# Performance work log

Hardware: AMD Instinct MI355X
Metric: run time of the kernel (lower is better)

Reference implementation:

```python
import jax, jax.numpy as jnp
import numpy as np

EMBED = 1024
HEADS = 16
HEAD_DIM = EMBED // HEADS


def setup_inputs() -> dict:
    key = jax.random.key(0)
    ks = jax.random.split(key, 9)
    s = 1.0 / np.sqrt(EMBED)
    inp = {
        "x": jax.random.normal(ks[0], (2, 2048, EMBED), dtype=jnp.float32),
        "wq": jax.random.uniform(ks[1], (EMBED, EMBED), jnp.float32, -s, s),
        "bq": jax.random.uniform(ks[2], (EMBED,), jnp.float32, -s, s),
        "wk": jax.random.uniform(ks[3], (EMBED, EMBED), jnp.float32, -s, s),
        "bk": jax.random.uniform(ks[4], (EMBED,), jnp.float32, -s, s),
        "wv": jax.random.uniform(ks[5], (EMBED, EMBED), jnp.float32, -s, s),
        "bv": jax.random.uniform(ks[6], (EMBED,), jnp.float32, -s, s),
        "wo": jax.random.uniform(ks[7], (EMBED, EMBED), jnp.float32, -s, s),
        "bo": jax.random.uniform(ks[8], (EMBED,), jnp.float32, -s, s),
    }
    return inp


def reference(x, wq, bq, wk, bk, wv, bv, wo, bo):
    B, S, E = x.shape
    H, D = HEADS, HEAD_DIM
    # projections (torch Linear: y = x @ W.T + b; here weights stored as [E, E] applied as x @ W.T)
    q = (x @ wq.T + bq).reshape(B, S, H, D).transpose(0, 2, 1, 3)  # [B,H,S,D]
    k = (x @ wk.T + bk).reshape(B, S, H, D).transpose(0, 2, 1, 3)
    v = (x @ wv.T + bv).reshape(B, S, H, D).transpose(0, 2, 1, 3)
    scores = jnp.einsum("bhqd,bhkd->bhqk", q, k) / jnp.sqrt(jnp.asarray(D, x.dtype))
    attn = jax.nn.softmax(scores, axis=-1)  # dropout is identity in eval / p=0
    ctx = jnp.einsum("bhqk,bhkd->bhqd", attn, v)
    ctx = ctx.transpose(0, 2, 1, 3).reshape(B, S, E)
    return ctx @ wo.T + bo
```

## Files before the change

kernel.cpp:

```cpp
#include <hip/hip_runtime.h>
#include <hip/hip_bf16.h>

#define EMBED 1024
#define HEADS 16
#define HDIM  64
#define BATCH 2
#define SEQ   2048
#define MTOT  (BATCH*SEQ)

typedef __attribute__((ext_vector_type(8))) short bf16x8;
typedef __attribute__((ext_vector_type(4))) short bf16x4;
typedef __attribute__((ext_vector_type(4))) float f32x4;
typedef __attribute__((ext_vector_type(8))) unsigned short u16x8;
typedef __attribute__((ext_vector_type(2))) unsigned u32x2;
typedef __attribute__((ext_vector_type(4))) unsigned u32x4;

__device__ __forceinline__ unsigned pack2(float lo, float hi) {
    __hip_bfloat162 h = __float22bfloat162_rn(make_float2(lo, hi));
    unsigned u;
    __builtin_memcpy(&u, &h, sizeof(u));
    return u;
}
__device__ __forceinline__ unsigned short f2bf(float f) {
    __hip_bfloat16 h = __float2bfloat16(f);
    unsigned short u;
    __builtin_memcpy(&u, &h, sizeof(u));
    return u;
}

__device__ __forceinline__ void glds16(const void* g, void* l) {
    __builtin_amdgcn_global_load_lds(
        (const __attribute__((address_space(1))) void*)g,
        (__attribute__((address_space(3))) void*)l, 16, 0, 0);
}

__global__ __launch_bounds__(256) void preconvert(
    const float* __restrict__ x,
    const float* __restrict__ wq, const float* __restrict__ wk,
    const float* __restrict__ wv, const float* __restrict__ wo,
    unsigned short* __restrict__ xb,
    unsigned short* __restrict__ wqb, unsigned short* __restrict__ wkb,
    unsigned short* __restrict__ wvb, unsigned short* __restrict__ wob)
{
    const int NX = (MTOT * EMBED) / 4;
    const int NW = (EMBED * EMBED) / 4;
    int idx = blockIdx.x * 256 + threadIdx.x;
    const float* src;
    unsigned short* dst;
    int off;
    if (idx < NX) {
        src = x; dst = xb; off = idx;
    } else {
        int r = idx - NX;
        int w = r / NW;
        off = r - w * NW;
        src = (w == 0) ? wq : (w == 1) ? wk : (w == 2) ? wv : wo;
        dst = (w == 0) ? wqb : (w == 1) ? wkb : (w == 2) ? wvb : wob;
    }
    float4 v = ((const float4*)src)[off];
    u32x2 o;
    o[0] = pack2(v.x, v.y);
    o[1] = pack2(v.z, v.w);
    *(u32x2*)(dst + (size_t)off * 4) = o;
}

__global__ __launch_bounds__(256, 2) void qkv_proj(
    const unsigned short* __restrict__ xb,
    const unsigned short* __restrict__ wqb, const float* __restrict__ bq,
    const unsigned short* __restrict__ wkb, const float* __restrict__ bk,
    const unsigned short* __restrict__ wvb, const float* __restrict__ bv,
    unsigned short* __restrict__ qo,
    unsigned short* __restrict__ ko,
    unsigned short* __restrict__ vto)
{
    const int which = blockIdx.z;
    const unsigned short* __restrict__ w =
        (which == 0) ? wqb : (which == 1) ? wkb : wvb;
    const float* __restrict__ bias = (which == 0) ? bq : (which == 1) ? bk : bv;
    const float kscale = (which == 1) ? 0.18033688f : 1.0f;

    const int m0 = blockIdx.x * 128;
    const int n0 = blockIdx.y * 128;

    __shared__ __align__(16) unsigned short a_lds[128 * 32];
    __shared__ __align__(16) unsigned short b_lds[128 * 32];

    const int tid  = threadIdx.x;
    const int lane = tid & 63;
    const int wid  = tid >> 6;
    const int wr   = wid >> 1, wc = wid & 1;
    const int lq   = lane & 15;
    const int lg   = lane >> 4;

    f32x4 acc[4][4] = {};

    const int srow  = wid * 32 + (lane >> 2);
    const int scol8 = (lane & 3) * 8;
    const unsigned short* ap0 = xb + (size_t)(m0 + srow)      * EMBED + scol8;
    const unsigned short* ap1 = xb + (size_t)(m0 + srow + 16) * EMBED + scol8;
    const unsigned short* bp0 = w  + (size_t)(n0 + srow)      * EMBED + scol8;
    const unsigned short* bp1 = w  + (size_t)(n0 + srow + 16) * EMBED + scol8;
    unsigned short* la0 = a_lds + wid * 1024;
    unsigned short* la1 = a_lds + wid * 1024 + 512;
    unsigned short* lb0 = b_lds + wid * 1024;
    unsigned short* lb1 = b_lds + wid * 1024 + 512;

    for (int k0 = 0; k0 < EMBED; k0 += 32) {
        glds16(ap0 + k0, la0);
        glds16(ap1 + k0, la1);
        glds16(bp0 + k0, lb0);
        glds16(bp1 + k0, lb1);
        __syncthreads();
        bf16x8 af[4], bfr[4];
        #pragma unroll
        for (int i = 0; i < 4; ++i)
            af[i] = *(const bf16x8*)&a_lds[(wr*64 + i*16 + lq) * 32 + lg*8];
        #pragma unroll
        for (int j = 0; j < 4; ++j)
            bfr[j] = *(const bf16x8*)&b_lds[(wc*64 + j*16 + lq) * 32 + lg*8];
        #pragma unroll
        for (int i = 0; i < 4; ++i)
            #pragma unroll
            for (int j = 0; j < 4; ++j)
                acc[i][j] = __builtin_amdgcn_mfma_f32_16x16x32_bf16(af[i], bfr[j], acc[i][j], 0, 0, 0);
        __syncthreads();
    }

    #pragma unroll
    for (int j = 0; j < 4; ++j) {
        const int nn = n0 + wc*64 + j*16 + lq;
        const float bsv = bias[nn];
        const int h = nn >> 6, d = nn & (HDIM-1);
        #pragma unroll
        for (int i = 0; i < 4; ++i) {
            const int mmb = m0 + wr*64 + i*16 + lg*4;
            const int b = mmb >> 11;
            const int s = mmb & (SEQ-1);
            const size_t bh = (size_t)(b*HEADS + h);
            if (which == 2) {
                u32x2 ov;
                ov[0] = pack2(acc[i][j][0] + bsv, acc[i][j][1] + bsv);
                ov[1] = pack2(acc[i][j][2] + bsv, acc[i][j][3] + bsv);
                *(u32x2*)&vto[(bh*HDIM + d)*SEQ + s] = ov;
            } else {
                unsigned short* o = (which == 0) ? qo : ko;
                #pragma unroll
                for (int r = 0; r < 4; ++r)
                    o[(bh*SEQ + (s + r))*HDIM + d] = f2bf((acc[i][j][r] + bsv) * kscale);
            }
        }
    }
}

__global__ __launch_bounds__(256, 4) void attn(
    const unsigned short* __restrict__ q,
    const unsigned short* __restrict__ k,
    const unsigned short* __restrict__ vt,
    unsigned short* __restrict__ ctx)
{
    __shared__ __align__(16) unsigned char sm[2 * 16384];

    const int bid   = blockIdx.x;
    const int xcd   = bid & 7;
    const int local = bid >> 3;
    const int bh    = xcd * 4 + (local >> 5);
    const int q0    = (local & 31) * 64;
    const int b     = bh >> 4;
    const int h     = bh & (HEADS - 1);
    const int tid   = threadIdx.x;
    const int wv    = tid >> 6;
    const int lane  = tid & 63;
    const int lq = lane & 15, lg = lane >> 4;

    const unsigned short* qb = q  + (size_t)bh * SEQ * HDIM;
    const unsigned short* kb = k  + (size_t)bh * SEQ * HDIM;
    const unsigned short* vb = vt + (size_t)bh * HDIM * SEQ;

    const int lg16 = lg * 16;
    const int Sp = (((lq & 3) | (((lq >> 2) & 1) << 2)) << 4);
    const int Tp = (((lq & 3) | (((lq >> 3) & 1) << 2)) << 4);
    const int kreadA = (8*(lq >> 2) + (lq & 3)) * 128 + (lg16 ^ Sp);
    const int kreadB = kreadA ^ 64;
    const int vreadA = lq * 128 + (lg16 ^ Tp);
    const int vreadB = vreadA ^ 64;

    const int wrow = tid >> 3;
    const int c8   = tid & 7;
    const int wS   = (((wrow & 3) | (((wrow >> 3) & 1) << 2)) << 4);
    const int woff = wrow * 128 + ((c8 * 16) ^ wS);

    const int scol = c8 * 8;
    const unsigned short* kp = kb + (size_t)wrow * HDIM + scol;
    const unsigned short* vp = vb + (size_t)wrow * SEQ + scol;

    bf16x8 qf[2];
    #pragma unroll
    for (int hh = 0; hh < 2; ++hh)
        qf[hh] = *(const bf16x8*)(qb + (size_t)(q0 + wv*16 + lq) * HDIM + hh*32 + lg*8);

    f32x4 o[4] = {};
    float lr = 0.f;

    u16x8 kr0, kr1, vr0, vr1;

#define LOADT() do {                                                           \
    kr0 = *(const u16x8*)(kp);                                                 \
    kr1 = *(const u16x8*)(kp + 32*HDIM);                                       \
    vr0 = *(const u16x8*)(vp);                                                 \
    vr1 = *(const u16x8*)(vp + 32*SEQ);                                        \
} while (0)

#define WRITET(BF) do {                                                        \
    unsigned char* smb = sm + (BF)*16384;                                      \
    *(u16x8*)(smb +         woff) = kr0;                                       \
    *(u16x8*)(smb +  4096 + woff) = kr1;                                       \
    *(u16x8*)(smb +  8192 + woff) = vr0;                                       \
    *(u16x8*)(smb + 12288 + woff) = vr1;                                       \
} while (0)

#define COMPUTE(BF) do {                                                       \
    const unsigned char* smb = sm + (BF)*16384;                                \
    f32x4 s_[4];                                                               \
    _Pragma("unroll")                                                          \
    for (int sub = 0; sub < 4; ++sub) {                                        \
        const int sadd = (sub & 1) * 512 + (sub >> 1) * 4096;                  \
        bf16x8 k0 = *(const bf16x8*)(smb + sadd + kreadA);                     \
        bf16x8 k1 = *(const bf16x8*)(smb + sadd + kreadB);                     \
        f32x4 z = {};                                                          \
        z = __builtin_amdgcn_mfma_f32_16x16x32_bf16(k0, qf[0], z, 0, 0, 0);    \
        z = __builtin_amdgcn_mfma_f32_16x16x32_bf16(k1, qf[1], z, 0, 0, 0);    \
        s_[sub] = z;                                                           \
    }                                                                          \
    u32x4 pbw0, pbw1;                                                          \
    float psum = 0.f;                                                          \
    _Pragma("unroll")                                                          \
    for (int sub = 0; sub < 4; ++sub) {                                        \
        f32x4 pv;                                                              \
        _Pragma("unroll")                                                      \
        for (int r = 0; r < 4; ++r) pv[r] = exp2f(s_[sub][r]);                 \
        psum += (pv[0] + pv[1]) + (pv[2] + pv[3]);                             \
        unsigned d0 = pack2(pv[0], pv[1]);                                     \
        unsigned d1 = pack2(pv[2], pv[3]);                                     \
        if (sub == 0)      { pbw0[0] = d0; pbw0[1] = d1; }                     \
        else if (sub == 1) { pbw0[2] = d0; pbw0[3] = d1; }                     \
        else if (sub == 2) { pbw1[0] = d0; pbw1[1] = d1; }                     \
        else               { pbw1[2] = d0; pbw1[3] = d1; }                     \
    }                                                                          \
    lr += psum;                                                                \
    bf16x8 pb0 = __builtin_bit_cast(bf16x8, pbw0);                             \
    bf16x8 pb1 = __builtin_bit_cast(bf16x8, pbw1);                             \
    _Pragma("unroll")                                                          \
    for (int i = 0; i < 4; ++i) {                                              \
        bf16x8 va = *(const bf16x8*)(smb + 8192 + i*2048 + vreadA);            \
        bf16x8 vbq = *(const bf16x8*)(smb + 8192 + i*2048 + vreadB);           \
        o[i] = __builtin_amdgcn_mfma_f32_16x16x32_bf16(va,  pb0, o[i], 0, 0, 0); \
        o[i] = __builtin_amdgcn_mfma_f32_16x16x32_bf16(vbq, pb1, o[i], 0, 0, 0); \
    }                                                                          \
} while (0)

    LOADT();
    WRITET(0);
    __syncthreads();
    kp += 64 * HDIM;
    vp += 64;

    for (int t2 = 0; t2 < 16; ++t2) {
        {
            const int t = 2 * t2;
            if (t < 31) LOADT();
            COMPUTE(0);
            if (t < 31) {
                WRITET(1);
                __syncthreads();
                kp += 64 * HDIM;
                vp += 64;
            }
        }
        {
            const int t = 2 * t2 + 1;
            if (t < 31) LOADT();
            COMPUTE(1);
            if (t < 31) {
                WRITET(0);
                __syncthreads();
                kp += 64 * HDIM;
                vp += 64;
            }
        }
    }

#undef LOADT
#undef WRITET
#undef COMPUTE

    float lm = lr + __shfl_xor(lr, 16);
    lm += __shfl_xor(lm, 32);
    const float inv = 1.0f / lm;
    unsigned short* cb = ctx + ((size_t)(b*SEQ + q0 + wv*16 + lq)) * EMBED + h*HDIM;
    #pragma unroll
    for (int i = 0; i < 4; ++i) {
        u32x2 ov;
        ov[0] = pack2(o[i][0] * inv, o[i][1] * inv);
        ov[1] = pack2(o[i][2] * inv, o[i][3] * inv);
        *(u32x2*)(cb + i*16 + lg*4) = ov;
    }
}

__global__ __launch_bounds__(256, 2) void out_proj(
    const unsigned short* __restrict__ ctx,
    const unsigned short* __restrict__ wob, const float* __restrict__ bo,
    float* __restrict__ out)
{
    const int m0 = blockIdx.x * 128;
    const int n0 = blockIdx.y * 128;

    __shared__ __align__(16) unsigned short a_lds[128 * 32];
    __shared__ __align__(16) unsigned short b_lds[128 * 32];

    const int tid  = threadIdx.x;
    const int lane = tid & 63;
    const int wid  = tid >> 6;
    const int wr   = wid >> 1, wc = wid & 1;
    const int lq   = lane & 15;
    const int lg   = lane >> 4;

    f32x4 acc[4][4] = {};

    const int srow  = wid * 32 + (lane >> 2);
    const int scol8 = (lane & 3) * 8;
    const unsigned short* ap0 = ctx + (size_t)(m0 + srow)      * EMBED + scol8;
    const unsigned short* ap1 = ctx + (size_t)(m0 + srow + 16) * EMBED + scol8;
    const unsigned short* bp0 = wob + (size_t)(n0 + srow)      * EMBED + scol8;
    const unsigned short* bp1 = wob + (size_t)(n0 + srow + 16) * EMBED + scol8;
    unsigned short* la0 = a_lds + wid * 1024;
    unsigned short* la1 = a_lds + wid * 1024 + 512;
    unsigned short* lb0 = b_lds + wid * 1024;
    unsigned short* lb1 = b_lds + wid * 1024 + 512;

    for (int k0 = 0; k0 < EMBED; k0 += 32) {
        glds16(ap0 + k0, la0);
        glds16(ap1 + k0, la1);
        glds16(bp0 + k0, lb0);
        glds16(bp1 + k0, lb1);
        __syncthreads();
        bf16x8 af[4], bfr[4];
        #pragma unroll
        for (int i = 0; i < 4; ++i)
            af[i] = *(const bf16x8*)&a_lds[(wr*64 + i*16 + lq) * 32 + lg*8];
        #pragma unroll
        for (int j = 0; j < 4; ++j)
            bfr[j] = *(const bf16x8*)&b_lds[(wc*64 + j*16 + lq) * 32 + lg*8];
        #pragma unroll
        for (int i = 0; i < 4; ++i)
            #pragma unroll
            for (int j = 0; j < 4; ++j)
                acc[i][j] = __builtin_amdgcn_mfma_f32_16x16x32_bf16(af[i], bfr[j], acc[i][j], 0, 0, 0);
        __syncthreads();
    }

    #pragma unroll
    for (int j = 0; j < 4; ++j) {
        const int nn = n0 + wc*64 + j*16 + lq;
        const float bsv = bo[nn];
        #pragma unroll
        for (int i = 0; i < 4; ++i) {
            const int mm = m0 + wr*64 + i*16 + lg*4;
            #pragma unroll
            for (int r = 0; r < 4; ++r)
                out[(size_t)(mm + r) * EMBED + nn] = acc[i][j][r] + bsv;
        }
    }
}

extern "C" void kernel_launch(void* const* d_in, const int* in_sizes, int n_in,
                              void* d_out, int out_size, void* d_ws, size_t ws_size,
                              hipStream_t stream) {
    const float* x  = (const float*)d_in[0];
    const float* wq = (const float*)d_in[1];
    const float* bq = (const float*)d_in[2];
    const float* wk = (const float*)d_in[3];
    const float* bk = (const float*)d_in[4];
    const float* wv = (const float*)d_in[5];
    const float* bv = (const float*)d_in[6];
    const float* wo = (const float*)d_in[7];
    const float* bo = (const float*)d_in[8];
    float* out = (float*)d_out;

    const size_t NELEM = (size_t)MTOT * EMBED;
    const size_t WELEM = (size_t)EMBED * EMBED;
    unsigned short* q_ws   = (unsigned short*)d_ws;
    unsigned short* k_ws   = q_ws  + NELEM;
    unsigned short* vt_ws  = k_ws  + NELEM;
    unsigned short* ctx_ws = vt_ws + NELEM;
    unsigned short* wqb    = ctx_ws + NELEM;
    unsigned short* wkb    = wqb + WELEM;
    unsigned short* wvb    = wkb + WELEM;
    unsigned short* wob    = wvb + WELEM;
    unsigned short* xb     = ctx_ws;

    const int NCONV = (int)((NELEM + 4 * WELEM) / 4);
    preconvert<<<dim3(NCONV / 256), 256, 0, stream>>>(
        x, wq, wk, wv, wo, xb, wqb, wkb, wvb, wob);
    qkv_proj<<<dim3(MTOT/128, EMBED/128, 3), 256, 0, stream>>>(
        xb, wqb, bq, wkb, bk, wvb, bv, q_ws, k_ws, vt_ws);
    attn<<<dim3(SEQ/64 * BATCH*HEADS), 256, 0, stream>>>(q_ws, k_ws, vt_ws, ctx_ws);
    out_proj<<<dim3(MTOT/128, EMBED/128), 256, 0, stream>>>(ctx_ws, wob, bo, out);
}
```

Measured before the change: 134.8 us.

## Process 128 queries per attention block and compute row sums with MFMA

```diff
diff --git a/kernel.cpp b/kernel.cpp
--- a/kernel.cpp
+++ b/kernel.cpp
@@ -152,7 +152,7 @@
     }
 }
 
-__global__ __launch_bounds__(256, 4) void attn(
+__global__ __launch_bounds__(256, 2) void attn(
     const unsigned short* __restrict__ q,
     const unsigned short* __restrict__ k,
     const unsigned short* __restrict__ vt,
@@ -163,8 +163,8 @@
     const int bid   = blockIdx.x;
     const int xcd   = bid & 7;
     const int local = bid >> 3;
-    const int bh    = xcd * 4 + (local >> 5);
-    const int q0    = (local & 31) * 64;
+    const int bh    = xcd * 4 + (local >> 4);
+    const int q0    = (local & 15) * 128;
     const int b     = bh >> 4;
     const int h     = bh & (HEADS - 1);
     const int tid   = threadIdx.x;
@@ -193,13 +193,20 @@
     const unsigned short* kp = kb + (size_t)wrow * HDIM + scol;
     const unsigned short* vp = vb + (size_t)wrow * SEQ + scol;
 
-    bf16x8 qf[2];
+    bf16x8 qf[2][2];
     #pragma unroll
-    for (int hh = 0; hh < 2; ++hh)
-        qf[hh] = *(const bf16x8*)(qb + (size_t)(q0 + wv*16 + lq) * HDIM + hh*32 + lg*8);
-
-    f32x4 o[4] = {};
-    float lr = 0.f;
+    for (int t = 0; t < 2; ++t)
+        #pragma unroll
+        for (int hh = 0; hh < 2; ++hh)
+            qf[t][hh] = *(const bf16x8*)(qb + (size_t)(q0 + wv*32 + t*16 + lq) * HDIM + hh*32 + lg*8);
+
+    u16x8 ones_u;
+    #pragma unroll
+    for (int e = 0; e < 8; ++e) ones_u[e] = 0x3F80;
+    const bf16x8 ones = __builtin_bit_cast(bf16x8, ones_u);
+
+    f32x4 o[2][4] = {};
+    f32x4 acc_l[2] = {};
 
     u16x8 kr0, kr1, vr0, vr1;
 
@@ -220,41 +227,50 @@
 
 #define COMPUTE(BF) do {                                                       \
     const unsigned char* smb = sm + (BF)*16384;                                \
-    f32x4 s_[4];                                                               \
+    f32x4 s_[2][4];                                                            \
     _Pragma("unroll")                                                          \
     for (int sub = 0; sub < 4; ++sub) {                                        \
         const int sadd = (sub & 1) * 512 + (sub >> 1) * 4096;                  \
         bf16x8 k0 = *(const bf16x8*)(smb + sadd + kreadA);                     \
         bf16x8 k1 = *(const bf16x8*)(smb + sadd + kreadB);                     \
-        f32x4 z = {};                                                          \
-        z = __builtin_amdgcn_mfma_f32_16x16x32_bf16(k0, qf[0], z, 0, 0, 0);    \
-        z = __builtin_amdgcn_mfma_f32_16x16x32_bf16(k1, qf[1], z, 0, 0, 0);    \
-        s_[sub] = z;                                                           \
+        _Pragma("unroll")                                                      \
+        for (int t = 0; t < 2; ++t) {                                          \
+            f32x4 z = {};                                                      \
+            z = __builtin_amdgcn_mfma_f32_16x16x32_bf16(k0, qf[t][0], z, 0, 0, 0); \
+            z = __builtin_amdgcn_mfma_f32_16x16x32_bf16(k1, qf[t][1], z, 0, 0, 0); \
+            s_[t][sub] = z;                                                    \
+        }                                                                      \
     }                                                                          \
-    u32x4 pbw0, pbw1;                                                          \
-    float psum = 0.f;                                                          \
+    bf16x8 pb[2][2];                                                           \
     _Pragma("unroll")                                                          \
-    for (int sub = 0; sub < 4; ++sub) {                                        \
-        f32x4 pv;                                                              \
+    for (int t = 0; t < 2; ++t) {                                              \
+        u32x4 pw0, pw1;                                                        \
         _Pragma("unroll")                                                      \
-        for (int r = 0; r < 4; ++r) pv[r] = exp2f(s_[sub][r]);                 \
-        psum += (pv[0] + pv[1]) + (pv[2] + pv[3]);                             \
-        unsigned d0 = pack2(pv[0], pv[1]);                                     \
-        unsigned d1 = pack2(pv[2], pv[3]);                                     \
-        if (sub == 0)      { pbw0[0] = d0; pbw0[1] = d1; }                     \
-        else if (sub == 1) { pbw0[2] = d0; pbw0[3] = d1; }                     \
-        else if (sub == 2) { pbw1[0] = d0; pbw1[1] = d1; }                     \
-        else               { pbw1[2] = d0; pbw1[3] = d1; }                     \
+        for (int sub = 0; sub < 4; ++sub) {                                    \
+            f32x4 pv;                                                          \
+            _Pragma("unroll")                                                  \
+            for (int r = 0; r < 4; ++r) pv[r] = exp2f(s_[t][sub][r]);          \
+            unsigned d0 = pack2(pv[0], pv[1]);                                 \
+            unsigned d1 = pack2(pv[2], pv[3]);                                 \
+            if (sub == 0)      { pw0[0] = d0; pw0[1] = d1; }                   \
+            else if (sub == 1) { pw0[2] = d0; pw0[3] = d1; }                   \
+            else if (sub == 2) { pw1[0] = d0; pw1[1] = d1; }                   \
+            else               { pw1[2] = d0; pw1[3] = d1; }                   \
+        }                                                                      \
+        pb[t][0] = __builtin_bit_cast(bf16x8, pw0);                            \
+        pb[t][1] = __builtin_bit_cast(bf16x8, pw1);                            \
+        acc_l[t] = __builtin_amdgcn_mfma_f32_16x16x32_bf16(ones, pb[t][0], acc_l[t], 0, 0, 0); \
+        acc_l[t] = __builtin_amdgcn_mfma_f32_16x16x32_bf16(ones, pb[t][1], acc_l[t], 0, 0, 0); \
     }                                                                          \
-    lr += psum;                                                                \
-    bf16x8 pb0 = __builtin_bit_cast(bf16x8, pbw0);                             \
-    bf16x8 pb1 = __builtin_bit_cast(bf16x8, pbw1);                             \
     _Pragma("unroll")                                                          \
     for (int i = 0; i < 4; ++i) {                                              \
-        bf16x8 va = *(const bf16x8*)(smb + 8192 + i*2048 + vreadA);            \
+        bf16x8 va  = *(const bf16x8*)(smb + 8192 + i*2048 + vreadA);           \
         bf16x8 vbq = *(const bf16x8*)(smb + 8192 + i*2048 + vreadB);           \
-        o[i] = __builtin_amdgcn_mfma_f32_16x16x32_bf16(va,  pb0, o[i], 0, 0, 0); \
-        o[i] = __builtin_amdgcn_mfma_f32_16x16x32_bf16(vbq, pb1, o[i], 0, 0, 0); \
+        _Pragma("unroll")                                                      \
+        for (int t = 0; t < 2; ++t) {                                          \
+            o[t][i] = __builtin_amdgcn_mfma_f32_16x16x32_bf16(va,  pb[t][0], o[t][i], 0, 0, 0); \
+            o[t][i] = __builtin_amdgcn_mfma_f32_16x16x32_bf16(vbq, pb[t][1], o[t][i], 0, 0, 0); \
+        }                                                                      \
     }                                                                          \
 } while (0)
 
@@ -293,16 +309,17 @@
 #undef WRITET
 #undef COMPUTE
 
-    float lm = lr + __shfl_xor(lr, 16);
-    lm += __shfl_xor(lm, 32);
-    const float inv = 1.0f / lm;
-    unsigned short* cb = ctx + ((size_t)(b*SEQ + q0 + wv*16 + lq)) * EMBED + h*HDIM;
     #pragma unroll
-    for (int i = 0; i < 4; ++i) {
-        u32x2 ov;
-        ov[0] = pack2(o[i][0] * inv, o[i][1] * inv);
-        ov[1] = pack2(o[i][2] * inv, o[i][3] * inv);
-        *(u32x2*)(cb + i*16 + lg*4) = ov;
+    for (int t = 0; t < 2; ++t) {
+        const float inv = 1.0f / acc_l[t][0];
+        unsigned short* cb = ctx + ((size_t)(b*SEQ + q0 + wv*32 + t*16 + lq)) * EMBED + h*HDIM;
+        #pragma unroll
+        for (int i = 0; i < 4; ++i) {
+            u32x2 ov;
+            ov[0] = pack2(o[t][i][0] * inv, o[t][i][1] * inv);
+            ov[1] = pack2(o[t][i][2] * inv, o[t][i][3] * inv);
+            *(u32x2*)(cb + i*16 + lg*4) = ov;
+        }
     }
 }
 
@@ -403,6 +420,6 @@
         x, wq, wk, wv, wo, xb, wqb, wkb, wvb, wob);
     qkv_proj<<<dim3(MTOT/128, EMBED/128, 3), 256, 0, stream>>>(
         xb, wqb, bq, wkb, bk, wvb, bv, q_ws, k_ws, vt_ws);
-    attn<<<dim3(SEQ/64 * BATCH*HEADS), 256, 0, stream>>>(q_ws, k_ws, vt_ws, ctx_ws);
+    attn<<<dim3((SEQ/128) * BATCH*HEADS), 256, 0, stream>>>(q_ws, k_ws, vt_ws, ctx_ws);
     out_proj<<<dim3(MTOT/128, EMBED/128), 256, 0, stream>>>(ctx_ws, wob, bo, out);
 }
```

After: 130.6 us. 1.03x faster.
